# Kernel tuning notes

Measured on AMD Instinct MI355X. Metric: run time of the kernel, lower is better.

Reference implementation:

```python
import jax, jax.numpy as jnp
import numpy as np

VAR_XY = 0.1  # SSD encoding variances
VAR_WH = 0.2


def _iou(truths, priors):
    # truths [G,4], priors [P,4] in corner form (x1,y1,x2,y2) -> [G,P]
    lt = jnp.maximum(truths[:, None, :2], priors[None, :, :2])
    rb = jnp.minimum(truths[:, None, 2:], priors[None, :, 2:])
    wh = jnp.clip(rb - lt, 0.0, None)
    inter = wh[..., 0] * wh[..., 1]
    area_t = (truths[:, 2] - truths[:, 0]) * (truths[:, 3] - truths[:, 1])
    area_p = (priors[:, 2] - priors[:, 0]) * (priors[:, 3] - priors[:, 1])
    return inter / (area_t[:, None] + area_p[None, :] - inter)


def _encode(truths, matched):
    # truths [G,1,4], matched priors [G,k,4], corner form -> SSD offsets [G,k,4]
    p_cxcy = (matched[..., :2] + matched[..., 2:]) * 0.5
    p_wh = matched[..., 2:] - matched[..., :2]
    g_cxcy = (truths[..., :2] + truths[..., 2:]) * 0.5
    g_wh = truths[..., 2:] - truths[..., :2]
    off_xy = (g_cxcy - p_cxcy) / (VAR_XY * p_wh)
    off_wh = jnp.log(g_wh / p_wh) / VAR_WH
    return jnp.concatenate([off_xy, off_wh], axis=-1)


def setup_inputs() -> dict:
    key = jax.random.key(0)
    k1, k2, k3, k4 = jax.random.split(key, 4)
    B, P, G = 16, 32768, 128
    # priors: valid corner-form boxes built from centers + sizes
    p_c = jax.random.uniform(k1, (B, P, 2), minval=0.1, maxval=0.9)
    p_s = jax.random.uniform(k2, (B, P, 2), minval=0.02, maxval=0.3)
    priors = jnp.concatenate([p_c - p_s * 0.5, p_c + p_s * 0.5], axis=-1)
    rpn_rois = jnp.stack([priors, priors], axis=1)  # [B,2,P,4]; channel 1 used
    # GT boxes, valid corner form
    t_c = jax.random.uniform(k3, (B, G, 2), minval=0.1, maxval=0.9)
    t_s = jax.random.uniform(k4, (B, G, 2), minval=0.05, maxval=0.4)
    targets = jnp.concatenate([t_c - t_s * 0.5, t_c + t_s * 0.5], axis=-1)
    return {"rpn_rois": rpn_rois, "targets": targets, "expand_num": 4}


def reference(rpn_rois, targets, expand_num):
    defaults = rpn_rois[:, 1]  # [B,P,4]

    def per_image(truths, priors):
        ious = _iou(truths, priors)                      # [G,P]
        _, idx = jax.lax.top_k(ious, expand_num)         # [G,k] best priors per GT
        matched = priors[idx]                            # [G,k,4]
        off = _encode(truths[:, None, :], matched)       # [G,k,4]
        return off.reshape(-1, 4)                        # [G*k,4]

    return jax.vmap(per_image)(targets, defaults)        # [B, G*k, 4]
```

## Files before the change

kernel.cpp:

```cpp
#include <hip/hip_runtime.h>

#define B 16
#define P 32768
#define NG 128
#define KTOP 4
#define TILE 256
#define NT (P / TILE)
#define SAMP 2048

typedef unsigned long long u64;
typedef unsigned int u32;

__device__ __forceinline__ void ceu(u64 &x, u64 &y) {
    u64 a = x, b = y; bool gt = a > b;
    x = gt ? a : b;  y = gt ? b : a;
}
__device__ __forceinline__ void cef(float &x, float &y) {
    float h = fmaxf(x, y), l = fminf(x, y); x = h; y = l;
}

#define INS4(x, a0, a1, a2, a3)                                   \
    {                                                             \
        bool g0 = (x) > a0, g1 = (x) > a1, g2 = (x) > a2, g3 = (x) > a3; \
        u64 n3 = g2 ? a2 : (g3 ? (x) : a3);                       \
        u64 n2 = g1 ? a1 : (g2 ? (x) : a2);                       \
        u64 n1 = g0 ? a0 : (g1 ? (x) : a1);                       \
        u64 n0 = g0 ? (x) : a0;                                   \
        a0 = n0; a1 = n1; a2 = n2; a3 = n3;                       \
    }

__global__ __launch_bounds__(256)
void k_tau(const float* __restrict__ rois, const float* __restrict__ targets,
           float* __restrict__ tau)
{
    #pragma clang fp contract(off)
    const int blk = blockIdx.x;
    const int b = blk >> 7, g = blk & (NG - 1);
    const int tid = threadIdx.x, lane = tid & 63, wv = tid >> 6;

    const float4 t = *(const float4*)(targets + ((size_t)(b * NG + g)) * 4);
    const float areaT = (t.z - t.x) * (t.w - t.y);
    const float4* __restrict__ pv = (const float4*)(rois + ((size_t)(2 * b + 1)) * P * 4);

    __shared__ float sf[4][4];
    float w0 = -1.f, w1 = -1.f, w2 = -1.f, w3 = -1.f;
    #pragma unroll
    for (int it = 0; it < SAMP / 256; ++it) {
        float4 q = pv[it * 256 + tid];
        float ap = (q.z - q.x) * (q.w - q.y);
        float ltx = fmaxf(t.x, q.x), lty = fmaxf(t.y, q.y);
        float rbx = fminf(t.z, q.z), rby = fminf(t.w, q.w);
        float wx = fmaxf(rbx - ltx, 0.0f);
        float wy = fmaxf(rby - lty, 0.0f);
        float inter = wx * wy;
        float iou = inter / ((areaT + ap) - inter);
        float x = iou, hh;
        hh = fmaxf(w0, x); x = fminf(w0, x); w0 = hh;
        hh = fmaxf(w1, x); x = fminf(w1, x); w1 = hh;
        hh = fmaxf(w2, x); x = fminf(w2, x); w2 = hh;
        w3 = fmaxf(w3, x);
    }
    #pragma unroll
    for (int d = 32; d >= 1; d >>= 1) {
        float n0 = __shfl_down(w0, d, 64);
        float n1 = __shfl_down(w1, d, 64);
        float n2 = __shfl_down(w2, d, 64);
        float n3 = __shfl_down(w3, d, 64);
        cef(w0, n3); cef(w1, n2); cef(w2, n1); cef(w3, n0);
        cef(w0, w2); cef(w1, w3); cef(w0, w1); cef(w2, w3);
    }
    if (lane == 0) { sf[wv][0] = w0; sf[wv][1] = w1; sf[wv][2] = w2; sf[wv][3] = w3; }
    __syncthreads();
    if (tid == 0) {
        float m0 = -1.f, m1 = -1.f, m2 = -1.f, m3 = -1.f;
        #pragma unroll
        for (int j = 0; j < 16; ++j) {
            float x = sf[j >> 2][j & 3], hh;
            hh = fmaxf(m0, x); x = fminf(m0, x); m0 = hh;
            hh = fmaxf(m1, x); x = fminf(m1, x); m1 = hh;
            hh = fmaxf(m2, x); x = fminf(m2, x); m2 = hh;
            m3 = fmaxf(m3, x);
        }
        tau[blk] = m3;
    }
}

__global__ __launch_bounds__(256, 4)
void k_scan(const float* __restrict__ rois, const float* __restrict__ targets,
            const float* __restrict__ tau, u64* __restrict__ part)
{
    #pragma clang fp contract(off)
    const int blk = blockIdx.x;
    const int b = blk / NT, tile = blk & (NT - 1);
    const int tid = threadIdx.x;
    const int g = tid & (NG - 1), hf = tid >> 7;

    __shared__ float4 sQ[TILE];
    __shared__ float  sA[TILE];
    __shared__ u64    sm[NG][4];

    const float4* __restrict__ pv =
        (const float4*)(rois + ((size_t)(2 * b + 1)) * P * 4) + (size_t)tile * TILE;
    {
        float4 q = pv[tid];
        sQ[tid] = q;
        sA[tid] = (q.z - q.x) * (q.w - q.y);
    }

    const float4 t = *(const float4*)(targets + ((size_t)(b * NG + g)) * 4);
    const float areaT = (t.z - t.x) * (t.w - t.y);
    const float tv    = tau[b * NG + g];
    const float slope = (tv / (1.0f + tv)) * (1.0f - 2e-4f);
    const float cA    = slope * areaT;
    __syncthreads();

    u64 a0 = 0, a1 = 0, a2 = 0, a3 = 0;
    const int base = hf * (TILE / 2);
    const u32 gidx = (u32)(tile * TILE + base);
    #pragma unroll 4
    for (int j = 0; j < TILE / 2; ++j) {
        const float4 q = sQ[base + j];
        const float ap = sA[base + j];
        float ltx = fmaxf(t.x, q.x), lty = fmaxf(t.y, q.y);
        float rbx = fminf(t.z, q.z), rby = fminf(t.w, q.w);
        float wx = fmaxf(rbx - ltx, 0.0f);
        float wy = fmaxf(rby - lty, 0.0f);
        float inter = wx * wy;
        bool pass = inter >= __builtin_fmaf(slope, ap, cA);
        if (__builtin_expect(__any(pass), 0)) {
            if (pass) {
                float iou = inter / ((areaT + ap) - inter);
                u64 x = ((u64)__float_as_uint(iou) << 32) | (u32)(~(gidx + (u32)j));
                INS4(x, a0, a1, a2, a3);
            }
        }
    }

    if (hf == 1) { sm[g][0] = a0; sm[g][1] = a1; sm[g][2] = a2; sm[g][3] = a3; }
    __syncthreads();
    if (hf == 0) {
        u64 b0 = sm[g][0], b1 = sm[g][1], b2 = sm[g][2], b3 = sm[g][3];
        ceu(a0, b3); ceu(a1, b2); ceu(a2, b1); ceu(a3, b0);
        ceu(a0, a2); ceu(a1, a3); ceu(a0, a1); ceu(a2, a3);
        u64* dst = part + (((size_t)b * NT + tile) * NG + g) * KTOP;
        dst[0] = a0; dst[1] = a1; dst[2] = a2; dst[3] = a3;
    }
}

__global__ __launch_bounds__(64)
void k_top(const float* __restrict__ rois, const float* __restrict__ targets,
           const u64* __restrict__ part, float* __restrict__ out)
{
    #pragma clang fp contract(off)
    const int blk = blockIdx.x;
    const int b = blk >> 7, g = blk & (NG - 1);
    const int lane = threadIdx.x;

    const u64* __restrict__ s0 = part + (((size_t)b * NT + lane) * NG + g) * KTOP;
    const u64* __restrict__ s1 = part + (((size_t)b * NT + lane + 64) * NG + g) * KTOP;
    u64 a0 = s0[0], a1 = s0[1], a2 = s0[2], a3 = s0[3];
    u64 b0 = s1[0], b1 = s1[1], b2 = s1[2], b3 = s1[3];
    ceu(a0, b3); ceu(a1, b2); ceu(a2, b1); ceu(a3, b0);
    ceu(a0, a2); ceu(a1, a3); ceu(a0, a1); ceu(a2, a3);
    #pragma unroll
    for (int d = 32; d >= 1; d >>= 1) {
        u64 n0 = __shfl_down(a0, d, 64);
        u64 n1 = __shfl_down(a1, d, 64);
        u64 n2 = __shfl_down(a2, d, 64);
        u64 n3 = __shfl_down(a3, d, 64);
        ceu(a0, n3); ceu(a1, n2); ceu(a2, n1); ceu(a3, n0);
        ceu(a0, a2); ceu(a1, a3); ceu(a0, a1); ceu(a2, a3);
    }
    if (lane == 0) {
        const float4 t = *(const float4*)(targets + ((size_t)(b * NG + g)) * 4);
        const float t0 = t.x, t1 = t.y, t2 = t.z, t3 = t.w;
        const float gw = t2 - t0, gh = t3 - t1;
        const float gcx = (t0 + t2) * 0.5f;
        const float gcy = (t1 + t3) * 0.5f;
        const float4* __restrict__ pv =
            (const float4*)(rois + ((size_t)(2 * b + 1)) * P * 4);
        float4* __restrict__ o4 = (float4*)out;

        u64 ks[KTOP] = {a0, a1, a2, a3};
        #pragma unroll
        for (int k = 0; k < KTOP; ++k) {
            int idx = (int)(~(u32)ks[k]) & (P - 1);
            float4 q = pv[idx];
            float pcx = (q.x + q.z) * 0.5f;
            float pcy = (q.y + q.w) * 0.5f;
            float pw  = q.z - q.x;
            float ph  = q.w - q.y;
            float4 r;
            r.x = (gcx - pcx) / (0.1f * pw);
            r.y = (gcy - pcy) / (0.1f * ph);
            r.z = logf(gw / pw) / 0.2f;
            r.w = logf(gh / ph) / 0.2f;
            o4[((size_t)(b * NG + g)) * KTOP + k] = r;
        }
    }
}

extern "C" void kernel_launch(void* const* d_in, const int* in_sizes, int n_in,
                              void* d_out, int out_size, void* d_ws, size_t ws_size,
                              hipStream_t stream) {
    const float* rois    = (const float*)d_in[0];
    const float* targets = (const float*)d_in[1];
    float* out = (float*)d_out;

    float* tau  = (float*)d_ws;
    u64*   part = (u64*)((char*)d_ws + 8192);

    k_tau <<<dim3(B * NG), dim3(256), 0, stream>>>(rois, targets, tau);
    k_scan<<<dim3(B * NT), dim3(256), 0, stream>>>(rois, targets, tau, part);
    k_top <<<dim3(B * NG), dim3(64),  0, stream>>>(rois, targets, part, out);
}
```

Measured before the change: 116.4 us.

## Split scan into branchless bitmask filter pass and sparse candidate processing

The scan loop no longer checks a wave-wide vote and branches on every prior. It first runs two fully unrolled passes that record which priors pass the threshold test as 64-bit masks per thread. It then revisits only the set bits to compute IoU and do the top-4 insertion, with the order of bits preserving the original tie-breaking. Launch bounds are raised to 8 waves per SIMD to push occupancy. The per-thread bit loops diverge across lanes, and the tighter register budget could cause spills.

New measurement: 122.4 us. 5.2% more time.

```diff
diff --git a/kernel.cpp b/kernel.cpp
--- a/kernel.cpp
+++ b/kernel.cpp
@@ -85,7 +85,7 @@
     }
 }
 
-__global__ __launch_bounds__(256, 4)
+__global__ __launch_bounds__(256, 8)
 void k_scan(const float* __restrict__ rois, const float* __restrict__ targets,
             const float* __restrict__ tau, u64* __restrict__ part)
 {
@@ -114,11 +114,11 @@
     const float cA    = slope * areaT;
     __syncthreads();
 
-    u64 a0 = 0, a1 = 0, a2 = 0, a3 = 0;
     const int base = hf * (TILE / 2);
-    const u32 gidx = (u32)(tile * TILE + base);
-    #pragma unroll 4
-    for (int j = 0; j < TILE / 2; ++j) {
+
+    u64 msk0 = 0, msk1 = 0;
+    #pragma unroll
+    for (int j = 0; j < 64; ++j) {
         const float4 q = sQ[base + j];
         const float ap = sA[base + j];
         float ltx = fmaxf(t.x, q.x), lty = fmaxf(t.y, q.y);
@@ -127,12 +127,41 @@
         float wy = fmaxf(rby - lty, 0.0f);
         float inter = wx * wy;
         bool pass = inter >= __builtin_fmaf(slope, ap, cA);
-        if (__builtin_expect(__any(pass), 0)) {
-            if (pass) {
-                float iou = inter / ((areaT + ap) - inter);
-                u64 x = ((u64)__float_as_uint(iou) << 32) | (u32)(~(gidx + (u32)j));
-                INS4(x, a0, a1, a2, a3);
-            }
+        msk0 |= ((u64)pass) << j;
+    }
+    #pragma unroll
+    for (int j = 0; j < 64; ++j) {
+        const float4 q = sQ[base + 64 + j];
+        const float ap = sA[base + 64 + j];
+        float ltx = fmaxf(t.x, q.x), lty = fmaxf(t.y, q.y);
+        float rbx = fminf(t.z, q.z), rby = fminf(t.w, q.w);
+        float wx = fmaxf(rbx - ltx, 0.0f);
+        float wy = fmaxf(rby - lty, 0.0f);
+        float inter = wx * wy;
+        bool pass = inter >= __builtin_fmaf(slope, ap, cA);
+        msk1 |= ((u64)pass) << j;
+    }
+
+    u64 a0 = 0, a1 = 0, a2 = 0, a3 = 0;
+    const u32 gbase = (u32)(tile * TILE + base);
+    #pragma clang loop unroll(disable)
+    for (int c = 0; c < 2; ++c) {
+        u64 m = c ? msk1 : msk0;
+        const int coff = c << 6;
+        while (m) {
+            int j = __builtin_ctzll(m);
+            m &= m - 1;
+            const int idx = base + coff + j;
+            const float4 q = sQ[idx];
+            const float ap = sA[idx];
+            float ltx = fmaxf(t.x, q.x), lty = fmaxf(t.y, q.y);
+            float rbx = fminf(t.z, q.z), rby = fminf(t.w, q.w);
+            float wx = fmaxf(rbx - ltx, 0.0f);
+            float wy = fmaxf(rby - lty, 0.0f);
+            float inter = wx * wy;
+            float iou = inter / ((areaT + ap) - inter);
+            u64 x = ((u64)__float_as_uint(iou) << 32) | (u32)(~(gbase + (u32)(coff + j)));
+            INS4(x, a0, a1, a2, a3);
         }
     }
 
```
